# Kernel tuning notes

Measured on AMD Instinct MI355X. Metric: run time of the kernel, lower is better.

## Reference

```python
import jax, jax.numpy as jnp
import numpy as np

N_NODES, N_EDGES, B = 5000, 160000, 8
IN_DIM, NB, RH = 64, 8, 64
MUL0, MUL1, MUL2 = 32, 16, 8
NW = 144  # 32*3 + 16*2 + 8*2 tensor-product path weights per edge
R_MAX, AVG_NEI = 6.0, 32.0
NL, POOL_H, OUT_D = 4, 128, 512


def setup_inputs():
    ks = jax.random.split(jax.random.key(0), 24)
    f = lambda k, shape, scale=1.0: jax.random.normal(k, shape, jnp.float32) * scale
    return {
        "x": f(ks[0], (N_NODES, IN_DIM)),
        "pos": f(ks[1], (N_NODES, 3)),
        "W_in": f(ks[2], (IN_DIM, MUL0), IN_DIM ** -0.5),
        "Wr1": f(ks[3], (NL, NB, RH), NB ** -0.5), "br1": jnp.zeros((NL, RH)),
        "Wr2": f(ks[4], (NL, RH, RH), RH ** -0.5), "br2": jnp.zeros((NL, RH)),
        "Wr3": f(ks[5], (NL, RH, NW), RH ** -0.5), "br3": jnp.zeros((NL, NW)),
        "Wm0": f(ks[6], (NL, 56, MUL0), 56 ** -0.5),
        "Wm1": f(ks[7], (NL, 48, MUL1), 48 ** -0.5),
        "Wm2": f(ks[8], (NL, 40, MUL2), 40 ** -0.5),
        "Ws0": f(ks[9], (NL, MUL0, MUL0), MUL0 ** -0.5),
        "Ws1": f(ks[10], (NL, MUL1, MUL1), MUL1 ** -0.5),
        "Ws2": f(ks[11], (NL, MUL2, MUL2), MUL2 ** -0.5),
        "Wg": f(ks[12], (NL, MUL0, MUL1 + MUL2), MUL0 ** -0.5), "bg": jnp.zeros((NL, MUL1 + MUL2)),
        "Wp1": f(ks[13], (MUL0, POOL_H), MUL0 ** -0.5), "bp1": jnp.zeros((POOL_H,)),
        "Wp2": f(ks[14], (POOL_H, POOL_H), POOL_H ** -0.5), "bp2": jnp.zeros((POOL_H,)),
        "Wp3": f(ks[15], (POOL_H, 1), POOL_H ** -0.5), "bp3": jnp.zeros((1,)),
        "Wo1": f(ks[16], (MUL0, OUT_D * 2), MUL0 ** -0.5), "bo1": jnp.zeros((OUT_D * 2,)),
        "g1": jnp.ones((OUT_D * 2,)), "be1": jnp.zeros((OUT_D * 2,)),
        "Wo2": f(ks[17], (OUT_D * 2, OUT_D), (OUT_D * 2) ** -0.5), "bo2": jnp.zeros((OUT_D,)),
        "g2": jnp.ones((OUT_D,)), "be2": jnp.zeros((OUT_D,)),
        "edge_index": jax.random.randint(ks[18], (2, N_EDGES), 0, N_NODES),
        "batch": jnp.sort(jax.random.randint(ks[19], (N_NODES,), 0, B)),
    }


def _ln(x, gamma, beta):
    m = x.mean(-1, keepdims=True)
    v = x.var(-1, keepdims=True)
    return (x - m) / jnp.sqrt(v + 1e-5) * gamma + beta


def _forward(x, pos, W_in, Wr1, br1, Wr2, br2, Wr3, br3, Wm0, Wm1, Wm2,
             Ws0, Ws1, Ws2, Wg, bg, Wp1, bp1, Wp2, bp2, Wp3, bp3,
             Wo1, bo1, g1, be1, Wo2, bo2, g2, be2, edge_index, batch):
    N = x.shape[0]
    src, dst = edge_index[0], edge_index[1]
    vec = pos[src] - pos[dst]                       # [E,3]
    r = jnp.sqrt(jnp.sum(vec * vec, -1) + 1e-12)    # [E]
    u = vec / r[:, None]
    # Bessel radial basis with smooth polynomial cutoff (p=6)
    nfreq = jnp.arange(1, NB + 1, dtype=x.dtype)
    bess = jnp.sqrt(2.0 / R_MAX) * jnp.sin(nfreq * jnp.pi * r[:, None] / R_MAX) / r[:, None]
    t = jnp.clip(r / R_MAX, 0.0, 1.0)
    fcut = (1.0 - 28.0 * t**6 + 48.0 * t**7 - 21.0 * t**8) * (r < R_MAX).astype(x.dtype)
    edge_emb = bess * fcut[:, None]                 # [E,NB]
    # real spherical harmonics of edge direction, component normalization
    ux, uy, uz = u[:, 0], u[:, 1], u[:, 2]
    Y1 = jnp.sqrt(3.0) * u                          # [E,3]
    Y2 = jnp.stack([15.0**0.5 * ux * uy, 15.0**0.5 * uy * uz,
                    0.5 * 5.0**0.5 * (3.0 * uz * uz - 1.0),
                    15.0**0.5 * ux * uz, 0.5 * 15.0**0.5 * (ux * ux - uy * uy)], -1)  # [E,5]
    # input embedding: 64x0e -> hidden irreps (only scalar path exists; l>0 start at 0)
    s = x @ W_in                                    # [N,32]
    v = jnp.zeros((N, MUL1, 3), x.dtype)            # [N,16,3] 1o
    q = jnp.zeros((N, MUL2, 5), x.dtype)            # [N,8,5]  2e
    for i in range(NL):
        w = jax.nn.silu(edge_emb @ Wr1[i] + br1[i])
        w = jax.nn.silu(w @ Wr2[i] + br2[i])
        w = w @ Wr3[i] + br3[i]                     # [E,144] per-edge TP path weights
        w_ss, w_sv, w_sq, w_vs, w_vv, w_qs, w_qq = jnp.split(w, [32, 64, 96, 112, 128, 136], -1)
        se, ve, qe = s[src], v[src], q[src]         # gather
        # tensor-product messages, grouped by output irrep
        m0 = jnp.concatenate([w_ss * se,
                              w_vv * jnp.einsum('ecm,em->ec', ve, Y1) / 3.0**0.5,
                              w_qq * jnp.einsum('ecm,em->ec', qe, Y2) / 5.0**0.5], -1)   # [E,56]
        m1 = jnp.concatenate([(w_sv * se)[:, :, None] * Y1[:, None, :],
                              w_vs[:, :, None] * ve], 1)                                  # [E,48,3]
        m2 = jnp.concatenate([(w_sq * se)[:, :, None] * Y2[:, None, :],
                              w_qs[:, :, None] * qe], 1)                                  # [E,40,5]
        a0 = jax.ops.segment_sum(m0, dst, num_segments=N) / AVG_NEI
        a1 = jax.ops.segment_sum(m1, dst, num_segments=N) / AVG_NEI
        a2 = jax.ops.segment_sum(m2, dst, num_segments=N) / AVG_NEI
        # per-irrep linear mix + self-connection
        ns = a0 @ Wm0[i] + s @ Ws0[i]
        nv = jnp.einsum('ncm,co->nom', a1, Wm1[i]) + jnp.einsum('ncm,co->nom', v, Ws1[i])
        nq = jnp.einsum('ncm,co->nom', a2, Wm2[i]) + jnp.einsum('ncm,co->nom', q, Ws2[i])
        # gate activation + resnet
        gates = jax.nn.sigmoid(ns @ Wg[i] + bg[i])  # [N,24]
        s = s + jax.nn.silu(ns)
        v = v + nv * gates[:, :MUL1, None]
        q = q + nq * gates[:, MUL1:, None]
    # attention pooling over scalar channels (scatter-softmax per graph)
    logits = (jax.nn.silu(jax.nn.silu(s @ Wp1 + bp1) @ Wp2 + bp2) @ Wp3 + bp3)[:, 0]
    mx = jax.ops.segment_max(logits, batch, num_segments=B)
    z = jnp.exp(logits - mx[batch])
    att = z / jax.ops.segment_sum(z, batch, num_segments=B)[batch]
    gpool = jax.ops.segment_sum(s * att[:, None], batch, num_segments=B)  # [B,32]
    h = jax.nn.silu(_ln(gpool @ Wo1 + bo1, g1, be1))
    return _ln(h @ Wo2 + bo2, g2, be2)              # [B,512]


def reference(x, pos, W_in, Wr1, br1, Wr2, br2, Wr3, br3, Wm0, Wm1, Wm2,
              Ws0, Ws1, Ws2, Wg, bg, Wp1, bp1, Wp2, bp2, Wp3, bp3,
              Wo1, bo1, g1, be1, Wo2, bo2, g2, be2, edge_index, batch):
    return _forward(x, pos, W_in, Wr1, br1, Wr2, br2, Wr3, br3, Wm0, Wm1, Wm2,
                    Ws0, Ws1, Ws2, Wg, bg, Wp1, bp1, Wp2, bp2, Wp3, bp3,
                    Wo1, bo1, g1, be1, Wo2, bo2, g2, be2, edge_index, batch)
```

## Files before the change

### kernel.cpp

```cpp
#include <hip/hip_runtime.h>

constexpr int NN  = 5000;
constexpr int NE  = 160000;
constexpr int NB_ = 8;
constexpr float RMAX   = 6.0f;
constexpr float INV_AVG = 1.0f/32.0f;
constexpr float SQ3  = 1.7320508075688772f;
constexpr float ISQ3 = 0.5773502691896258f;
constexpr float ISQ5 = 0.4472135954999579f;
constexpr float SQ15 = 3.872983346207417f;
constexpr float SQ5  = 2.2360679774997896f;
constexpr float PIF  = 3.14159265358979323846f;

__device__ __forceinline__ float sigmoid_f(float x){
    return 1.0f / (1.0f + __expf(-x));
}
__device__ __forceinline__ float silu_f(float x){ return x * sigmoid_f(x); }

__global__ void k_geom(const float* __restrict__ pos, const int* __restrict__ ei,
                       float* __restrict__ geom, int* __restrict__ counts){
    int e = blockIdx.x*256 + threadIdx.x;
    if (e >= NE) return;
    int s = ei[e], d = ei[NE + e];
    float vx = pos[3*s]-pos[3*d], vy = pos[3*s+1]-pos[3*d+1], vz = pos[3*s+2]-pos[3*d+2];
    float r2 = vx*vx + vy*vy + vz*vz + 1e-12f;
    float r  = sqrtf(r2);
    float ir = 1.0f/r;
    float ux = vx*ir, uy = vy*ir, uz = vz*ir;
    float t  = fminf(r*(1.0f/RMAX), 1.0f);
    float t2=t*t, t3=t2*t, t6=t3*t3, t7=t6*t, t8=t7*t;
    float fc = (1.0f - 28.0f*t6 + 48.0f*t7 - 21.0f*t8) * (r < RMAX ? 1.0f : 0.0f);
    float cb = sqrtf(2.0f/RMAX) * ir * fc;
    float w[16];
    #pragma unroll
    for (int k=0;k<8;k++){
        float arg = (float)(k+1) * (PIF/RMAX) * r;
        w[k] = cb * sinf(arg);
    }
    w[8]  = SQ3*ux; w[9] = SQ3*uy; w[10] = SQ3*uz;
    w[11] = SQ15*ux*uy; w[12] = SQ15*uy*uz; w[13] = 0.5f*SQ5*(3.0f*uz*uz-1.0f);
    w[14] = SQ15*ux*uz; w[15] = 0.5f*SQ15*(ux*ux-uy*uy);
    float4* o = (float4*)(geom + (size_t)e*16);
    o[0] = make_float4(w[0],w[1],w[2],w[3]);
    o[1] = make_float4(w[4],w[5],w[6],w[7]);
    o[2] = make_float4(w[8],w[9],w[10],w[11]);
    o[3] = make_float4(w[12],w[13],w[14],w[15]);
    atomicAdd(&counts[d], 1);
}

__global__ void k_scan(int* __restrict__ cr, int* __restrict__ fpos){
    __shared__ int part[256];
    int t = threadIdx.x;
    const int CH = (NN + 255)/256;
    int base = t*CH;
    int s = 0;
    for (int i=0;i<CH;i++){ int idx = base+i; if (idx < NN) s += cr[idx]; }
    part[t] = s; __syncthreads();
    for (int off=1; off<256; off<<=1){
        int v = (t >= off) ? part[t-off] : 0;
        __syncthreads();
        part[t] += v;
        __syncthreads();
    }
    int run = (t==0) ? 0 : part[t-1];
    for (int i=0;i<CH;i++){
        int idx = base+i;
        if (idx < NN){
            int c = cr[idx];
            cr[idx]  = run;
            fpos[idx] = run;
            run += c;
        } else if (idx == NN){
            cr[idx] = run;
        }
    }
}

__global__ void k_fill(const int* __restrict__ ei, int* __restrict__ fpos,
                       int* __restrict__ elist, int* __restrict__ slot){
    int e = blockIdx.x*256 + threadIdx.x;
    if (e >= NE) return;
    int d = ei[NE+e];
    int p = atomicAdd(&fpos[d], 1);
    elist[p] = e;
    slot[e]  = p;
}

__global__ void k_sinit(const float* __restrict__ x, const float* __restrict__ Win,
                        float* __restrict__ sA){
    int tid = blockIdx.x*256 + threadIdx.x;
    int n = tid >> 5, o = tid & 31;
    if (n >= NN) return;
    float a = 0.f;
    #pragma unroll
    for (int k=0;k<64;k++) a = fmaf(x[n*64+k], Win[k*32+o], a);
    sA[n*32+o] = a;
}

__launch_bounds__(256)
__global__ void k_mlp(const float* __restrict__ geom, const int* __restrict__ slot,
                      const float* __restrict__ Wr1, const float* __restrict__ br1,
                      const float* __restrict__ Wr2, const float* __restrict__ br2,
                      const float* __restrict__ Wr3, const float* __restrict__ br3,
                      float* __restrict__ wbuf, int layer){
    __shared__ float w1s[8*64];
    __shared__ float w2s[64*64];
    __shared__ float w3s[64*144];
    __shared__ float b1s[64], b2s[64], b3s[144];
    __shared__ float embs[64][8];
    __shared__ float hs[64][68];
    __shared__ int   slots[64];

    const int t  = threadIdx.x;
    const int e0 = blockIdx.x * 64;
    const float* W1 = Wr1 + layer*(8*64);
    const float* b1 = br1 + layer*64;
    const float* W2 = Wr2 + layer*(64*64);
    const float* b2 = br2 + layer*64;
    const float* W3 = Wr3 + layer*(64*144);
    const float* b3 = br3 + layer*144;

    {
        const float4* W2v = (const float4*)W2;
        float4* w2v = (float4*)w2s;
        #pragma unroll
        for (int i=0;i<4;i++) w2v[t + 256*i] = W2v[t + 256*i];
        const float4* W3v = (const float4*)W3;
        float4* w3v = (float4*)w3s;
        #pragma unroll
        for (int i=0;i<9;i++) w3v[t + 256*i] = W3v[t + 256*i];
        if (t < 128) ((float4*)w1s)[t] = ((const float4*)W1)[t];
        if (t < 64){ b1s[t] = b1[t]; b2s[t] = b2[t]; slots[t] = slot[e0 + t]; }
        if (t < 144) b3s[t] = b3[t];
        if (t < 128){
            ((float4*)embs)[t] = *((const float4*)geom + (size_t)(e0 + (t>>1))*4 + (t&1));
        }
    }
    __syncthreads();

    const int eg = t >> 3;
    const int jg = t & 7;
    const int ea = eg*2, eb = ea+1;

    float a0[2][8];
    #pragma unroll
    for (int i=0;i<2;i++)
        #pragma unroll
        for (int u=0;u<8;u++) a0[i][u] = b1s[8*jg+u];
    #pragma unroll
    for (int k=0;k<8;k++){
        float e_a = embs[ea][k], e_b = embs[eb][k];
        #pragma unroll
        for (int u=0;u<8;u++){
            float wv = w1s[k*64 + 8*jg + u];
            a0[0][u] = fmaf(e_a, wv, a0[0][u]);
            a0[1][u] = fmaf(e_b, wv, a0[1][u]);
        }
    }
    #pragma unroll
    for (int i=0;i<2;i++){
        int e = ea + i;
        float4 p0 = make_float4(silu_f(a0[i][0]), silu_f(a0[i][1]), silu_f(a0[i][2]), silu_f(a0[i][3]));
        float4 p1 = make_float4(silu_f(a0[i][4]), silu_f(a0[i][5]), silu_f(a0[i][6]), silu_f(a0[i][7]));
        *(float4*)&hs[e][8*jg]     = p0;
        *(float4*)&hs[e][8*jg + 4] = p1;
    }
    __syncthreads();

    float a1[2][8];
    #pragma unroll
    for (int i=0;i<2;i++)
        #pragma unroll
        for (int u=0;u<8;u++) a1[i][u] = b2s[8*jg+u];
    #pragma unroll
    for (int k=0;k<64;k++){
        float h_a = hs[ea][k], h_b = hs[eb][k];
        float4 wA = *(const float4*)&w2s[k*64 + 8*jg];
        float4 wB = *(const float4*)&w2s[k*64 + 8*jg + 4];
        a1[0][0]=fmaf(h_a,wA.x,a1[0][0]); a1[0][1]=fmaf(h_a,wA.y,a1[0][1]);
        a1[0][2]=fmaf(h_a,wA.z,a1[0][2]); a1[0][3]=fmaf(h_a,wA.w,a1[0][3]);
        a1[0][4]=fmaf(h_a,wB.x,a1[0][4]); a1[0][5]=fmaf(h_a,wB.y,a1[0][5]);
        a1[0][6]=fmaf(h_a,wB.z,a1[0][6]); a1[0][7]=fmaf(h_a,wB.w,a1[0][7]);
        a1[1][0]=fmaf(h_b,wA.x,a1[1][0]); a1[1][1]=fmaf(h_b,wA.y,a1[1][1]);
        a1[1][2]=fmaf(h_b,wA.z,a1[1][2]); a1[1][3]=fmaf(h_b,wA.w,a1[1][3]);
        a1[1][4]=fmaf(h_b,wB.x,a1[1][4]); a1[1][5]=fmaf(h_b,wB.y,a1[1][5]);
        a1[1][6]=fmaf(h_b,wB.z,a1[1][6]); a1[1][7]=fmaf(h_b,wB.w,a1[1][7]);
    }
    __syncthreads();
    #pragma unroll
    for (int i=0;i<2;i++){
        int e = ea + i;
        float4 p0 = make_float4(silu_f(a1[i][0]), silu_f(a1[i][1]), silu_f(a1[i][2]), silu_f(a1[i][3]));
        float4 p1 = make_float4(silu_f(a1[i][4]), silu_f(a1[i][5]), silu_f(a1[i][6]), silu_f(a1[i][7]));
        *(float4*)&hs[e][8*jg]     = p0;
        *(float4*)&hs[e][8*jg + 4] = p1;
    }
    __syncthreads();

    float c2[2][18];
    #pragma unroll
    for (int i=0;i<2;i++)
        #pragma unroll
        for (int u=0;u<18;u++) c2[i][u] = b3s[18*jg+u];
    #pragma unroll
    for (int k=0;k<64;k++){
        float h_a = hs[ea][k], h_b = hs[eb][k];
        #pragma unroll
        for (int u2=0;u2<9;u2++){
            float2 wv = *(const float2*)&w3s[k*144 + 18*jg + 2*u2];
            c2[0][2*u2]   = fmaf(h_a, wv.x, c2[0][2*u2]);
            c2[0][2*u2+1] = fmaf(h_a, wv.y, c2[0][2*u2+1]);
            c2[1][2*u2]   = fmaf(h_b, wv.x, c2[1][2*u2]);
            c2[1][2*u2+1] = fmaf(h_b, wv.y, c2[1][2*u2+1]);
        }
    }
    #pragma unroll
    for (int i=0;i<2;i++){
        float* wo = wbuf + (size_t)slots[ea+i]*144 + 18*jg;
        #pragma unroll
        for (int u2=0;u2<9;u2++)
            *(float2*)(wo + 2*u2) = make_float2(c2[i][2*u2], c2[i][2*u2+1]);
    }
}

__launch_bounds__(64)
__global__ void k_gather(const int* __restrict__ rowp, const int* __restrict__ elist,
                         const int* __restrict__ ei, const float* __restrict__ geom,
                         const float* __restrict__ wbuf,
                         const float* __restrict__ s_in, const float* __restrict__ v_in,
                         const float* __restrict__ q_in,
                         float* __restrict__ s_out, float* __restrict__ v_out,
                         float* __restrict__ q_out,
                         const float* __restrict__ Wm0, const float* __restrict__ Wm1,
                         const float* __restrict__ Wm2,
                         const float* __restrict__ Ws0, const float* __restrict__ Ws1,
                         const float* __restrict__ Ws2,
                         const float* __restrict__ Wg, const float* __restrict__ bg,
                         int layer){
    constexpr int SH_W = 0, SH_Y = 144, SH_SE = 152, SH_VE = 184, SH_QE = 232, SH_ONE = 272;
    __shared__ float sh[273];
    __shared__ float lacc[400];
    __shared__ float lnode[120];
    __shared__ float lns[32];
    __shared__ float lgate[24];
    int n = blockIdx.x;
    int lane = threadIdx.x;
    if (lane < 32) lnode[lane]      = s_in[n*32+lane];
    if (lane < 48) lnode[32+lane]   = v_in[n*48+lane];
    if (lane < 40) lnode[80+lane]   = q_in[n*40+lane];
    if (lane == 0) sh[SH_ONE] = 1.0f;

    int typ[7], wiA[7], siA[7], yiA[7];
    #pragma unroll
    for (int t=0;t<7;t++){
        int c = lane + 64*t;
        int T=3, W=0, S=0, Y=SH_ONE;
        if (c < 32){ T=0; W=c; S=SH_SE+c; }
        else if (c < 48){ T=1; W=112+(c-32); S=SH_VE+3*(c-32); }
        else if (c < 56){ T=2; W=136+(c-48); S=SH_QE+5*(c-48); }
        else if (c < 200){
            int d=c-56; int row=d/3; int col=d-3*row;
            if (row < 32){ T=0; W=32+row;       S=SH_SE+row;              Y=SH_Y+col; }
            else         { T=0; W=96+(row-32);  S=SH_VE+3*(row-32)+col; }
        } else if (c < 400){
            int d=c-200; int row=d/5; int col=d-5*row;
            if (row < 32){ T=0; W=64+row;       S=SH_SE+row;              Y=SH_Y+3+col; }
            else         { T=0; W=128+(row-32); S=SH_QE+5*(row-32)+col; }
        }
        typ[t]=T; wiA[t]=W; siA[t]=S; yiA[t]=Y;
    }
    float acc[7];
    #pragma unroll
    for (int t=0;t<7;t++) acc[t]=0.f;

    int beg = rowp[n], end = rowp[n+1];
    for (int idx=beg; idx<end; ++idx){
        int e   = elist[idx];
        int src = ei[e];
        if (lane < 36){
            *(float4*)&sh[SH_W + lane*4] = *(const float4*)(wbuf + (size_t)idx*144 + lane*4);
        } else if (lane < 38){
            *(float4*)&sh[SH_Y + (lane-36)*4] = *(const float4*)(geom + (size_t)e*16 + 8 + (lane-36)*4);
        } else if (lane < 46){
            *(float4*)&sh[SH_SE + (lane-38)*4] = *(const float4*)(s_in + (size_t)src*32 + (lane-38)*4);
        } else if (lane < 58){
            *(float4*)&sh[SH_VE + (lane-46)*4] = *(const float4*)(v_in + (size_t)src*48 + (lane-46)*4);
        } else {
            *(float4*)&sh[SH_QE + (lane-58)*4] = *(const float4*)(q_in + (size_t)src*40 + (lane-58)*4);
        }
        if (lane < 4){
            *(float4*)&sh[SH_QE + 24 + lane*4] = *(const float4*)(q_in + (size_t)src*40 + 24 + lane*4);
        }
        __syncthreads();
        #pragma unroll
        for (int t=0;t<7;t++){
            float m;
            if (typ[t]==0)      m = sh[wiA[t]] * sh[siA[t]] * sh[yiA[t]];
            else if (typ[t]==1) m = sh[wiA[t]] * ISQ3 *
                                    (sh[siA[t]]*sh[SH_Y] + sh[siA[t]+1]*sh[SH_Y+1] + sh[siA[t]+2]*sh[SH_Y+2]);
            else if (typ[t]==2) m = sh[wiA[t]] * ISQ5 *
                                    (sh[siA[t]]*sh[SH_Y+3] + sh[siA[t]+1]*sh[SH_Y+4] + sh[siA[t]+2]*sh[SH_Y+5] +
                                     sh[siA[t]+3]*sh[SH_Y+6] + sh[siA[t]+4]*sh[SH_Y+7]);
            else                m = 0.f;
            acc[t] += m;
        }
        __syncthreads();
    }
    #pragma unroll
    for (int t=0;t<7;t++){
        int c = lane + 64*t;
        if (c < 400) lacc[c] = acc[t] * INV_AVG;
    }
    __syncthreads();

    const float* Wm0p = Wm0 + layer*(56*32);
    const float* Ws0p = Ws0 + layer*(32*32);
    const float* Wm1p = Wm1 + layer*(48*16);
    const float* Ws1p = Ws1 + layer*(16*16);
    const float* Wm2p = Wm2 + layer*(40*8);
    const float* Ws2p = Ws2 + layer*(8*8);
    const float* Wgp  = Wg  + layer*(32*24);
    const float* bgp  = bg  + layer*24;

    if (lane < 32){
        float a = 0.f;
        #pragma unroll
        for (int c=0;c<56;c++) a = fmaf(lacc[c],  Wm0p[c*32+lane], a);
        #pragma unroll
        for (int c=0;c<32;c++) a = fmaf(lnode[c], Ws0p[c*32+lane], a);
        lns[lane] = a;
    }
    int o3 = lane/3, m3 = lane - 3*o3;
    int o5 = lane/5, m5 = lane - 5*o5;
    float nv = 0.f, nq = 0.f;
    if (lane < 48){
        float a = 0.f;
        #pragma unroll
        for (int c=0;c<48;c++) a = fmaf(lacc[56+c*3+m3],   Wm1p[c*16+o3], a);
        #pragma unroll
        for (int c=0;c<16;c++) a = fmaf(lnode[32+c*3+m3],  Ws1p[c*16+o3], a);
        nv = a;
    }
    if (lane < 40){
        float a = 0.f;
        #pragma unroll
        for (int c=0;c<40;c++) a = fmaf(lacc[200+c*5+m5],  Wm2p[c*8+o5], a);
        #pragma unroll
        for (int c=0;c<8;c++)  a = fmaf(lnode[80+c*5+m5],  Ws2p[c*8+o5], a);
        nq = a;
    }
    __syncthreads();
    if (lane < 24){
        float a = bgp[lane];
        #pragma unroll
        for (int c=0;c<32;c++) a = fmaf(lns[c], Wgp[c*24+lane], a);
        lgate[lane] = sigmoid_f(a);
    }
    __syncthreads();
    if (lane < 32) s_out[n*32+lane] = lnode[lane]    + silu_f(lns[lane]);
    if (lane < 48) v_out[n*48+lane] = lnode[32+lane] + nv * lgate[o3];
    if (lane < 40) q_out[n*40+lane] = lnode[80+lane] + nq * lgate[16+o5];
}

__launch_bounds__(128)
__global__ void k_pool(const float* __restrict__ s_in,
                       const float* __restrict__ Wp1, const float* __restrict__ bp1,
                       const float* __restrict__ Wp2, const float* __restrict__ bp2,
                       const float* __restrict__ Wp3, const float* __restrict__ bp3,
                       float* __restrict__ logits){
    __shared__ float ls[32];
    __shared__ float lh[128];
    __shared__ float wred[2];
    int n = blockIdx.x, t = threadIdx.x;
    if (t < 32) ls[t] = s_in[n*32+t];
    __syncthreads();
    float a = bp1[t];
    #pragma unroll
    for (int c=0;c<32;c++) a = fmaf(ls[c], Wp1[c*128+t], a);
    lh[t] = silu_f(a);
    __syncthreads();
    float b = bp2[t];
    #pragma unroll
    for (int k=0;k<128;k++) b = fmaf(lh[k], Wp2[k*128+t], b);
    float p = silu_f(b) * Wp3[t];
    #pragma unroll
    for (int off=32; off>0; off>>=1) p += __shfl_down(p, off, 64);
    if ((t & 63) == 0) wred[t>>6] = p;
    __syncthreads();
    if (t == 0) logits[n] = wred[0] + wred[1] + bp3[0];
}

__global__ void k_bmax(const float* __restrict__ logits, const int* __restrict__ batch,
                       float* __restrict__ mx){
    __shared__ float red[256];
    int b = blockIdx.x, t = threadIdx.x;
    float m = -3.0e38f;
    for (int n=t; n<NN; n+=256) if (batch[n]==b) m = fmaxf(m, logits[n]);
    red[t] = m; __syncthreads();
    for (int s2=128; s2>0; s2>>=1){ if (t<s2) red[t] = fmaxf(red[t], red[t+s2]); __syncthreads(); }
    if (t==0) mx[b] = red[0];
}

__global__ void k_z(const float* __restrict__ logits, const int* __restrict__ batch,
                    const float* __restrict__ mx, float* __restrict__ zbuf,
                    float* __restrict__ denom){
    int n = blockIdx.x*256 + threadIdx.x;
    if (n >= NN) return;
    int b = batch[n];
    float z = __expf(logits[n] - mx[b]);
    zbuf[n] = z;
    atomicAdd(&denom[b], z);
}

__global__ void k_gpool(const float* __restrict__ s_in, const float* __restrict__ zbuf,
                        const int* __restrict__ batch, const float* __restrict__ denom,
                        float* __restrict__ gpool){
    __shared__ float red[8][32];
    int b = blockIdx.x, t = threadIdx.x;
    int c = t & 31, g = t >> 5;
    float a = 0.f;
    for (int n=g; n<NN; n+=8){
        if (batch[n]==b) a = fmaf(zbuf[n], s_in[n*32+c], a);
    }
    red[g][c] = a; __syncthreads();
    if (t < 32){
        float s2 = 0.f;
        #pragma unroll
        for (int g2=0; g2<8; g2++) s2 += red[g2][t];
        gpool[b*32+t] = s2 / denom[b];
    }
}

__launch_bounds__(1024)
__global__ void k_out1(const float* __restrict__ gpool, const float* __restrict__ Wo1,
                       const float* __restrict__ bo1, const float* __restrict__ g1,
                       const float* __restrict__ be1, float* __restrict__ hbuf){
    __shared__ float lg[32];
    __shared__ float red[1024];
    __shared__ float stats[2];
    int b = blockIdx.x, t = threadIdx.x;
    if (t < 32) lg[t] = gpool[b*32+t];
    __syncthreads();
    float a = bo1[t];
    #pragma unroll
    for (int c=0;c<32;c++) a = fmaf(lg[c], Wo1[c*1024+t], a);
    red[t] = a; __syncthreads();
    for (int s2=512; s2>0; s2>>=1){ if (t<s2) red[t]+=red[t+s2]; __syncthreads(); }
    if (t==0) stats[0] = red[0]*(1.0f/1024.0f);
    __syncthreads();
    float mean = stats[0];
    float d = a - mean;
    red[t] = d*d; __syncthreads();
    for (int s2=512; s2>0; s2>>=1){ if (t<s2) red[t]+=red[t+s2]; __syncthreads(); }
    if (t==0) stats[1] = red[0]*(1.0f/1024.0f);
    __syncthreads();
    float rstd = rsqrtf(stats[1] + 1e-5f);
    hbuf[b*1024+t] = silu_f(d*rstd*g1[t] + be1[t]);
}

__launch_bounds__(1024)
__global__ void k_out2(const float* __restrict__ hbuf, const float* __restrict__ Wo2,
                       const float* __restrict__ bo2, const float* __restrict__ g2,
                       const float* __restrict__ be2, float* __restrict__ out){
    __shared__ float lh[1024];
    __shared__ float part[1024];
    __shared__ float red[1024];
    __shared__ float stats[2];
    int b = blockIdx.x, t = threadIdx.x;
    lh[t] = hbuf[b*1024 + t];
    __syncthreads();
    int j = t & 511, half = t >> 9;
    float a = (half == 0) ? bo2[j] : 0.0f;
    int k0 = half*512;
    #pragma unroll 8
    for (int k=0;k<512;k++) a = fmaf(lh[k0+k], Wo2[(size_t)(k0+k)*512 + j], a);
    part[t] = a; __syncthreads();
    float y = 0.f;
    if (t < 512) y = part[t] + part[t+512];
    red[t] = (t < 512) ? y : 0.f; __syncthreads();
    for (int s2=512; s2>0; s2>>=1){ if (t<s2) red[t]+=red[t+s2]; __syncthreads(); }
    if (t==0) stats[0] = red[0]*(1.0f/512.0f);
    __syncthreads();
    float mean = stats[0];
    float d = y - mean;
    red[t] = (t < 512) ? d*d : 0.f; __syncthreads();
    for (int s2=512; s2>0; s2>>=1){ if (t<s2) red[t]+=red[t+s2]; __syncthreads(); }
    if (t==0) stats[1] = red[0]*(1.0f/512.0f);
    __syncthreads();
    float rstd = rsqrtf(stats[1] + 1e-5f);
    if (t < 512) out[b*512+t] = d*rstd*g2[t] + be2[t];
}

extern "C" void kernel_launch(void* const* d_in, const int* in_sizes, int n_in,
                              void* d_out, int out_size, void* d_ws, size_t ws_size,
                              hipStream_t stream){
    const float* x   = (const float*)d_in[0];
    const float* pos = (const float*)d_in[1];
    const float* Win = (const float*)d_in[2];
    const float* Wr1 = (const float*)d_in[3];
    const float* br1 = (const float*)d_in[4];
    const float* Wr2 = (const float*)d_in[5];
    const float* br2 = (const float*)d_in[6];
    const float* Wr3 = (const float*)d_in[7];
    const float* br3 = (const float*)d_in[8];
    const float* Wm0 = (const float*)d_in[9];
    const float* Wm1 = (const float*)d_in[10];
    const float* Wm2 = (const float*)d_in[11];
    const float* Ws0 = (const float*)d_in[12];
    const float* Ws1 = (const float*)d_in[13];
    const float* Ws2 = (const float*)d_in[14];
    const float* Wg  = (const float*)d_in[15];
    const float* bg  = (const float*)d_in[16];
    const float* Wp1 = (const float*)d_in[17];
    const float* bp1 = (const float*)d_in[18];
    const float* Wp2 = (const float*)d_in[19];
    const float* bp2 = (const float*)d_in[20];
    const float* Wp3 = (const float*)d_in[21];
    const float* bp3 = (const float*)d_in[22];
    const float* Wo1 = (const float*)d_in[23];
    const float* bo1 = (const float*)d_in[24];
    const float* g1  = (const float*)d_in[25];
    const float* be1 = (const float*)d_in[26];
    const float* Wo2 = (const float*)d_in[27];
    const float* bo2 = (const float*)d_in[28];
    const float* g2  = (const float*)d_in[29];
    const float* be2 = (const float*)d_in[30];
    const int* ei    = (const int*)d_in[31];
    const int* batch = (const int*)d_in[32];
    float* out = (float*)d_out;

    char* wsb = (char*)d_ws;
    size_t off = 0;
    auto take = [&](size_t bytes)->char*{
        char* p = wsb + off;
        off = (off + bytes + 255) & ~(size_t)255;
        return p;
    };
    float* geom  = (float*)take((size_t)NE*16*4);
    float* wbuf  = (float*)take((size_t)NE*144*4);
    int*   rowp  = (int*)take((size_t)(NN+1)*4);
    int*   fpos  = (int*)take((size_t)NN*4);
    int*   elist = (int*)take((size_t)NE*4);
    int*   slot  = (int*)take((size_t)NE*4);
    float* sA = (float*)take((size_t)NN*32*4);
    float* sB = (float*)take((size_t)NN*32*4);
    float* vA = (float*)take((size_t)NN*48*4);
    float* vB = (float*)take((size_t)NN*48*4);
    float* qA = (float*)take((size_t)NN*40*4);
    float* qB = (float*)take((size_t)NN*40*4);
    float* logits = (float*)take((size_t)NN*4);
    float* zbuf   = (float*)take((size_t)NN*4);
    float* mx     = (float*)take(64);
    float* denom  = (float*)take(64);
    float* gpool  = (float*)take((size_t)NB_*32*4);
    float* hbuf   = (float*)take((size_t)NB_*1024*4);
    (void)ws_size; (void)in_sizes; (void)n_in; (void)out_size;

    hipMemsetAsync(rowp, 0, (size_t)(NN+1)*4, stream);
    hipMemsetAsync(vA,   0, (size_t)NN*48*4, stream);
    hipMemsetAsync(qA,   0, (size_t)NN*40*4, stream);
    hipMemsetAsync(denom,0, 64, stream);

    k_geom<<<(NE+255)/256, 256, 0, stream>>>(pos, ei, geom, rowp);
    k_scan<<<1, 256, 0, stream>>>(rowp, fpos);
    k_fill<<<(NE+255)/256, 256, 0, stream>>>(ei, fpos, elist, slot);
    k_sinit<<<(NN*32+255)/256, 256, 0, stream>>>(x, Win, sA);

    float* si=sA; float* so=sB; float* vi=vA; float* vo=vB; float* qi=qA; float* qo=qB;
    for (int layer=0; layer<4; ++layer){
        k_mlp<<<NE/64, 256, 0, stream>>>(geom, slot, Wr1, br1, Wr2, br2, Wr3, br3, wbuf, layer);
        k_gather<<<NN, 64, 0, stream>>>(rowp, elist, ei, geom, wbuf, si, vi, qi, so, vo, qo,
                                        Wm0, Wm1, Wm2, Ws0, Ws1, Ws2, Wg, bg, layer);
        float* ts=si; si=so; so=ts;
        float* tv=vi; vi=vo; vo=tv;
        float* tq=qi; qi=qo; qo=tq;
    }
    k_pool<<<NN, 128, 0, stream>>>(si, Wp1, bp1, Wp2, bp2, Wp3, bp3, logits);
    k_bmax<<<NB_, 256, 0, stream>>>(logits, batch, mx);
    k_z<<<(NN+255)/256, 256, 0, stream>>>(logits, batch, mx, zbuf, denom);
    k_gpool<<<NB_, 256, 0, stream>>>(si, zbuf, batch, denom, gpool);
    k_out1<<<NB_, 1024, 0, stream>>>(gpool, Wo1, bo1, g1, be1, hbuf);
    k_out2<<<NB_, 1024, 0, stream>>>(hbuf, Wo2, bo2, g2, be2, out);
}
```

Baseline: 1.147 ms.

## Parallelize gather over four waves, stream W3 from global, use batch ranges for pooling

The per-node gather kernel now uses 256 threads, with four waves each taking every fourth incoming edge. Each lane computes its tensor-product paths straight from global memory, and the partial sums are reduced in shared memory. This removes the per-edge shared staging and the two barriers per edge. The edge MLP's last layer now reads W3 from global/L1 with one edge per four threads instead of staging 36KB in shared memory, which should raise occupancy. Segment ranges are precomputed from the sorted batch so the max and pooling kernels scan only their own segment, at the cost of an extra small kernel.

```diff
diff --git a/kernel.cpp b/kernel.cpp
--- a/kernel.cpp
+++ b/kernel.cpp
@@ -97,7 +97,7 @@
     sA[n*32+o] = a;
 }
 
-__launch_bounds__(256)
+__launch_bounds__(256, 4)
 __global__ void k_mlp(const float* __restrict__ geom, const int* __restrict__ slot,
                       const float* __restrict__ Wr1, const float* __restrict__ br1,
                       const float* __restrict__ Wr2, const float* __restrict__ br2,
@@ -105,8 +105,7 @@
                       float* __restrict__ wbuf, int layer){
     __shared__ float w1s[8*64];
     __shared__ float w2s[64*64];
-    __shared__ float w3s[64*144];
-    __shared__ float b1s[64], b2s[64], b3s[144];
+    __shared__ float b1s[64], b2s[64];
     __shared__ float embs[64][8];
     __shared__ float hs[64][68];
     __shared__ int   slots[64];
@@ -125,13 +124,8 @@
         float4* w2v = (float4*)w2s;
         #pragma unroll
         for (int i=0;i<4;i++) w2v[t + 256*i] = W2v[t + 256*i];
-        const float4* W3v = (const float4*)W3;
-        float4* w3v = (float4*)w3s;
-        #pragma unroll
-        for (int i=0;i<9;i++) w3v[t + 256*i] = W3v[t + 256*i];
         if (t < 128) ((float4*)w1s)[t] = ((const float4*)W1)[t];
         if (t < 64){ b1s[t] = b1[t]; b2s[t] = b2[t]; slots[t] = slot[e0 + t]; }
-        if (t < 144) b3s[t] = b3[t];
         if (t < 128){
             ((float4*)embs)[t] = *((const float4*)geom + (size_t)(e0 + (t>>1))*4 + (t&1));
         }
@@ -197,33 +191,38 @@
     }
     __syncthreads();
 
-    float c2[2][18];
-    #pragma unroll
-    for (int i=0;i<2;i++)
-        #pragma unroll
-        for (int u=0;u<18;u++) c2[i][u] = b3s[18*jg+u];
-    #pragma unroll
+    const int et = t >> 2;
+    const int cg = t & 3;
+    float c4[36];
+    {
+        const float4* b3v = (const float4*)(b3 + 36*cg);
+        #pragma unroll
+        for (int u4=0;u4<9;u4++){
+            float4 bv = b3v[u4];
+            c4[4*u4]=bv.x; c4[4*u4+1]=bv.y; c4[4*u4+2]=bv.z; c4[4*u4+3]=bv.w;
+        }
+    }
+    const float* W3c = W3 + 36*cg;
+    #pragma unroll 4
     for (int k=0;k<64;k++){
-        float h_a = hs[ea][k], h_b = hs[eb][k];
-        #pragma unroll
-        for (int u2=0;u2<9;u2++){
-            float2 wv = *(const float2*)&w3s[k*144 + 18*jg + 2*u2];
-            c2[0][2*u2]   = fmaf(h_a, wv.x, c2[0][2*u2]);
-            c2[0][2*u2+1] = fmaf(h_a, wv.y, c2[0][2*u2+1]);
-            c2[1][2*u2]   = fmaf(h_b, wv.x, c2[1][2*u2]);
-            c2[1][2*u2+1] = fmaf(h_b, wv.y, c2[1][2*u2+1]);
-        }
-    }
-    #pragma unroll
-    for (int i=0;i<2;i++){
-        float* wo = wbuf + (size_t)slots[ea+i]*144 + 18*jg;
-        #pragma unroll
-        for (int u2=0;u2<9;u2++)
-            *(float2*)(wo + 2*u2) = make_float2(c2[i][2*u2], c2[i][2*u2+1]);
-    }
-}
-
-__launch_bounds__(64)
+        float h = hs[et][k];
+        const float4* wr = (const float4*)(W3c + k*144);
+        #pragma unroll
+        for (int u4=0;u4<9;u4++){
+            float4 wv = wr[u4];
+            c4[4*u4]   = fmaf(h, wv.x, c4[4*u4]);
+            c4[4*u4+1] = fmaf(h, wv.y, c4[4*u4+1]);
+            c4[4*u4+2] = fmaf(h, wv.z, c4[4*u4+2]);
+            c4[4*u4+3] = fmaf(h, wv.w, c4[4*u4+3]);
+        }
+    }
+    float* wo = wbuf + (size_t)slots[et]*144 + 36*cg;
+    #pragma unroll
+    for (int u4=0;u4<9;u4++)
+        *(float4*)(wo + 4*u4) = make_float4(c4[4*u4], c4[4*u4+1], c4[4*u4+2], c4[4*u4+3]);
+}
+
+__launch_bounds__(256, 8)
 __global__ void k_gather(const int* __restrict__ rowp, const int* __restrict__ elist,
                          const int* __restrict__ ei, const float* __restrict__ geom,
                          const float* __restrict__ wbuf,
@@ -237,80 +236,110 @@
                          const float* __restrict__ Ws2,
                          const float* __restrict__ Wg, const float* __restrict__ bg,
                          int layer){
-    constexpr int SH_W = 0, SH_Y = 144, SH_SE = 152, SH_VE = 184, SH_QE = 232, SH_ONE = 272;
-    __shared__ float sh[273];
+    __shared__ float pacc[4][400];
     __shared__ float lacc[400];
-    __shared__ float lnode[120];
     __shared__ float lns[32];
     __shared__ float lgate[24];
-    int n = blockIdx.x;
-    int lane = threadIdx.x;
-    if (lane < 32) lnode[lane]      = s_in[n*32+lane];
-    if (lane < 48) lnode[32+lane]   = v_in[n*48+lane];
-    if (lane < 40) lnode[80+lane]   = q_in[n*40+lane];
-    if (lane == 0) sh[SH_ONE] = 1.0f;
-
-    int typ[7], wiA[7], siA[7], yiA[7];
-    #pragma unroll
-    for (int t=0;t<7;t++){
-        int c = lane + 64*t;
-        int T=3, W=0, S=0, Y=SH_ONE;
-        if (c < 32){ T=0; W=c; S=SH_SE+c; }
-        else if (c < 48){ T=1; W=112+(c-32); S=SH_VE+3*(c-32); }
-        else if (c < 56){ T=2; W=136+(c-48); S=SH_QE+5*(c-48); }
-        else if (c < 200){
-            int d=c-56; int row=d/3; int col=d-3*row;
-            if (row < 32){ T=0; W=32+row;       S=SH_SE+row;              Y=SH_Y+col; }
-            else         { T=0; W=96+(row-32);  S=SH_VE+3*(row-32)+col; }
-        } else if (c < 400){
-            int d=c-200; int row=d/5; int col=d-5*row;
-            if (row < 32){ T=0; W=64+row;       S=SH_SE+row;              Y=SH_Y+3+col; }
-            else         { T=0; W=128+(row-32); S=SH_QE+5*(row-32)+col; }
-        }
-        typ[t]=T; wiA[t]=W; siA[t]=S; yiA[t]=Y;
-    }
-    float acc[7];
-    #pragma unroll
-    for (int t=0;t<7;t++) acc[t]=0.f;
-
-    int beg = rowp[n], end = rowp[n+1];
-    for (int idx=beg; idx<end; ++idx){
+    const int n = blockIdx.x;
+    const int t = threadIdx.x;
+    const int w = t >> 6;
+    const int lane = t & 63;
+
+    int s0_w, s0_o, s0_ob;
+    if (lane < 32){ s0_w = lane;            s0_o = lane;          s0_ob = lane; }
+    else if (lane < 48){ s0_w = 112+(lane-32); s0_o = 3*(lane-32); s0_ob = lane; }
+    else if (lane < 56){ s0_w = 136+(lane-48); s0_o = 5*(lane-48); s0_ob = lane; }
+    else { int R = lane-56; s0_w = 32+R; s0_o = R; s0_ob = 56+3*R; }
+    int s1_w, s1_o, s1_ob;
+    if (lane < 24){ int R = lane+8; s1_w = 32+R; s1_o = R;     s1_ob = 56+3*R; }
+    else if (lane < 40){ int j = lane-24; s1_w = 96+j; s1_o = 3*j; s1_ob = 152+3*j; }
+    else { int R = lane-40; s1_w = 64+R; s1_o = R; s1_ob = 200+5*R; }
+    int s2_w, s2_o, s2_ob;
+    if (lane < 8){ int R = lane+24; s2_w = 64+R; s2_o = R;   s2_ob = 200+5*R; }
+    else { int j = lane-8; s2_w = 128+j; s2_o = 5*j; s2_ob = 360+5*j; }
+
+    float a0[3] = {0.f,0.f,0.f};
+    float a1[5] = {0.f,0.f,0.f,0.f,0.f};
+    float a2[5] = {0.f,0.f,0.f,0.f,0.f};
+
+    const int beg = rowp[n], end = rowp[n+1];
+    for (int idx = beg + w; idx < end; idx += 4){
         int e   = elist[idx];
         int src = ei[e];
-        if (lane < 36){
-            *(float4*)&sh[SH_W + lane*4] = *(const float4*)(wbuf + (size_t)idx*144 + lane*4);
-        } else if (lane < 38){
-            *(float4*)&sh[SH_Y + (lane-36)*4] = *(const float4*)(geom + (size_t)e*16 + 8 + (lane-36)*4);
-        } else if (lane < 46){
-            *(float4*)&sh[SH_SE + (lane-38)*4] = *(const float4*)(s_in + (size_t)src*32 + (lane-38)*4);
-        } else if (lane < 58){
-            *(float4*)&sh[SH_VE + (lane-46)*4] = *(const float4*)(v_in + (size_t)src*48 + (lane-46)*4);
-        } else {
-            *(float4*)&sh[SH_QE + (lane-58)*4] = *(const float4*)(q_in + (size_t)src*40 + (lane-58)*4);
-        }
-        if (lane < 4){
-            *(float4*)&sh[SH_QE + 24 + lane*4] = *(const float4*)(q_in + (size_t)src*40 + 24 + lane*4);
-        }
-        __syncthreads();
-        #pragma unroll
-        for (int t=0;t<7;t++){
-            float m;
-            if (typ[t]==0)      m = sh[wiA[t]] * sh[siA[t]] * sh[yiA[t]];
-            else if (typ[t]==1) m = sh[wiA[t]] * ISQ3 *
-                                    (sh[siA[t]]*sh[SH_Y] + sh[siA[t]+1]*sh[SH_Y+1] + sh[siA[t]+2]*sh[SH_Y+2]);
-            else if (typ[t]==2) m = sh[wiA[t]] * ISQ5 *
-                                    (sh[siA[t]]*sh[SH_Y+3] + sh[siA[t]+1]*sh[SH_Y+4] + sh[siA[t]+2]*sh[SH_Y+5] +
-                                     sh[siA[t]+3]*sh[SH_Y+6] + sh[siA[t]+4]*sh[SH_Y+7]);
-            else                m = 0.f;
-            acc[t] += m;
-        }
-        __syncthreads();
-    }
-    #pragma unroll
-    for (int t=0;t<7;t++){
-        int c = lane + 64*t;
-        if (c < 400) lacc[c] = acc[t] * INV_AVG;
-    }
+        const float* gp = geom + (size_t)e*16;
+        float4 y14 = *(const float4*)(gp + 8);
+        float4 y58 = *(const float4*)(gp + 12);
+        const float* wp = wbuf + (size_t)idx*144;
+        const float* sp = s_in + (size_t)src*32;
+        const float* vp = v_in + (size_t)src*48;
+        const float* qp = q_in + (size_t)src*40;
+        {
+            float wv = wp[s0_w];
+            if (lane < 32){
+                a0[0] = fmaf(wv, sp[s0_o], a0[0]);
+            } else if (lane < 48){
+                float dv = vp[s0_o]*y14.x + vp[s0_o+1]*y14.y + vp[s0_o+2]*y14.z;
+                a0[0] = fmaf(wv*ISQ3, dv, a0[0]);
+            } else if (lane < 56){
+                float dq = qp[s0_o]*y14.w + qp[s0_o+1]*y58.x + qp[s0_o+2]*y58.y
+                         + qp[s0_o+3]*y58.z + qp[s0_o+4]*y58.w;
+                a0[0] = fmaf(wv*ISQ5, dq, a0[0]);
+            } else {
+                float tmp = wv * sp[s0_o];
+                a0[0] = fmaf(tmp, y14.x, a0[0]);
+                a0[1] = fmaf(tmp, y14.y, a0[1]);
+                a0[2] = fmaf(tmp, y14.z, a0[2]);
+            }
+        }
+        {
+            float wv = wp[s1_w];
+            if (lane < 24){
+                float tmp = wv * sp[s1_o];
+                a1[0] = fmaf(tmp, y14.x, a1[0]);
+                a1[1] = fmaf(tmp, y14.y, a1[1]);
+                a1[2] = fmaf(tmp, y14.z, a1[2]);
+            } else if (lane < 40){
+                a1[0] = fmaf(wv, vp[s1_o],   a1[0]);
+                a1[1] = fmaf(wv, vp[s1_o+1], a1[1]);
+                a1[2] = fmaf(wv, vp[s1_o+2], a1[2]);
+            } else {
+                float tmp = wv * sp[s1_o];
+                a1[0] = fmaf(tmp, y14.w, a1[0]);
+                a1[1] = fmaf(tmp, y58.x, a1[1]);
+                a1[2] = fmaf(tmp, y58.y, a1[2]);
+                a1[3] = fmaf(tmp, y58.z, a1[3]);
+                a1[4] = fmaf(tmp, y58.w, a1[4]);
+            }
+        }
+        if (lane < 16){
+            float wv = wp[s2_w];
+            if (lane < 8){
+                float tmp = wv * sp[s2_o];
+                a2[0] = fmaf(tmp, y14.w, a2[0]);
+                a2[1] = fmaf(tmp, y58.x, a2[1]);
+                a2[2] = fmaf(tmp, y58.y, a2[2]);
+                a2[3] = fmaf(tmp, y58.z, a2[3]);
+                a2[4] = fmaf(tmp, y58.w, a2[4]);
+            } else {
+                a2[0] = fmaf(wv, qp[s2_o],   a2[0]);
+                a2[1] = fmaf(wv, qp[s2_o+1], a2[1]);
+                a2[2] = fmaf(wv, qp[s2_o+2], a2[2]);
+                a2[3] = fmaf(wv, qp[s2_o+3], a2[3]);
+                a2[4] = fmaf(wv, qp[s2_o+4], a2[4]);
+            }
+        }
+    }
+    pacc[w][s0_ob] = a0[0];
+    if (lane >= 56){ pacc[w][s0_ob+1] = a0[1]; pacc[w][s0_ob+2] = a0[2]; }
+    pacc[w][s1_ob] = a1[0]; pacc[w][s1_ob+1] = a1[1]; pacc[w][s1_ob+2] = a1[2];
+    if (lane >= 40){ pacc[w][s1_ob+3] = a1[3]; pacc[w][s1_ob+4] = a1[4]; }
+    if (lane < 16){
+        #pragma unroll
+        for (int u=0;u<5;u++) pacc[w][s2_ob+u] = a2[u];
+    }
+    __syncthreads();
+    for (int c=t; c<400; c+=256)
+        lacc[c] = (pacc[0][c]+pacc[1][c]+pacc[2][c]+pacc[3][c]) * INV_AVG;
     __syncthreads();
 
     const float* Wm0p = Wm0 + layer*(56*32);
@@ -322,44 +351,44 @@
     const float* Wgp  = Wg  + layer*(32*24);
     const float* bgp  = bg  + layer*24;
 
-    if (lane < 32){
+    float nvv = 0.f, nqv = 0.f;
+    if (t < 32){
         float a = 0.f;
         #pragma unroll
-        for (int c=0;c<56;c++) a = fmaf(lacc[c],  Wm0p[c*32+lane], a);
-        #pragma unroll
-        for (int c=0;c<32;c++) a = fmaf(lnode[c], Ws0p[c*32+lane], a);
-        lns[lane] = a;
-    }
-    int o3 = lane/3, m3 = lane - 3*o3;
-    int o5 = lane/5, m5 = lane - 5*o5;
-    float nv = 0.f, nq = 0.f;
-    if (lane < 48){
-        float a = 0.f;
-        #pragma unroll
-        for (int c=0;c<48;c++) a = fmaf(lacc[56+c*3+m3],   Wm1p[c*16+o3], a);
-        #pragma unroll
-        for (int c=0;c<16;c++) a = fmaf(lnode[32+c*3+m3],  Ws1p[c*16+o3], a);
-        nv = a;
-    }
-    if (lane < 40){
-        float a = 0.f;
-        #pragma unroll
-        for (int c=0;c<40;c++) a = fmaf(lacc[200+c*5+m5],  Wm2p[c*8+o5], a);
-        #pragma unroll
-        for (int c=0;c<8;c++)  a = fmaf(lnode[80+c*5+m5],  Ws2p[c*8+o5], a);
-        nq = a;
-    }
-    __syncthreads();
-    if (lane < 24){
-        float a = bgp[lane];
-        #pragma unroll
-        for (int c=0;c<32;c++) a = fmaf(lns[c], Wgp[c*24+lane], a);
-        lgate[lane] = sigmoid_f(a);
-    }
-    __syncthreads();
-    if (lane < 32) s_out[n*32+lane] = lnode[lane]    + silu_f(lns[lane]);
-    if (lane < 48) v_out[n*48+lane] = lnode[32+lane] + nv * lgate[o3];
-    if (lane < 40) q_out[n*40+lane] = lnode[80+lane] + nq * lgate[16+o5];
+        for (int c=0;c<56;c++) a = fmaf(lacc[c], Wm0p[c*32+t], a);
+        #pragma unroll
+        for (int c=0;c<32;c++) a = fmaf(s_in[n*32+c], Ws0p[c*32+t], a);
+        lns[t] = a;
+    } else if (t >= 64 && t < 112){
+        int o = t-64, o3 = o/3, m3 = o-3*o3;
+        #pragma unroll
+        for (int c=0;c<48;c++) nvv = fmaf(lacc[56+c*3+m3], Wm1p[c*16+o3], nvv);
+        #pragma unroll
+        for (int c=0;c<16;c++) nvv = fmaf(v_in[n*48+c*3+m3], Ws1p[c*16+o3], nvv);
+    } else if (t >= 128 && t < 168){
+        int o = t-128, o5 = o/5, m5 = o-5*o5;
+        #pragma unroll
+        for (int c=0;c<40;c++) nqv = fmaf(lacc[200+c*5+m5], Wm2p[c*8+o5], nqv);
+        #pragma unroll
+        for (int c=0;c<8;c++)  nqv = fmaf(q_in[n*40+c*5+m5], Ws2p[c*8+o5], nqv);
+    }
+    __syncthreads();
+    if (t < 24){
+        float a = bgp[t];
+        #pragma unroll
+        for (int c=0;c<32;c++) a = fmaf(lns[c], Wgp[c*24+t], a);
+        lgate[t] = sigmoid_f(a);
+    }
+    __syncthreads();
+    if (t < 32){
+        s_out[n*32+t] = s_in[n*32+t] + silu_f(lns[t]);
+    } else if (t >= 64 && t < 112){
+        int o = t-64;
+        v_out[n*48+o] = v_in[n*48+o] + nvv * lgate[o/3];
+    } else if (t >= 128 && t < 168){
+        int o = t-128;
+        q_out[n*40+o] = q_in[n*40+o] + nqv * lgate[16+o/5];
+    }
 }
 
 __launch_bounds__(128)
@@ -390,14 +419,24 @@
     if (t == 0) logits[n] = wred[0] + wred[1] + bp3[0];
 }
 
-__global__ void k_bmax(const float* __restrict__ logits, const int* __restrict__ batch,
-                       float* __restrict__ mx){
-    __shared__ float red[256];
+__global__ void k_ranges(const int* __restrict__ batch, int* __restrict__ rs, int* __restrict__ re){
+    int n = blockIdx.x*256 + threadIdx.x;
+    if (n >= NN) return;
+    int b = batch[n];
+    if (n == 0 || batch[n-1] != b) rs[b] = n;
+    if (n == NN-1 || batch[n+1] != b) re[b] = n+1;
+}
+
+__launch_bounds__(1024)
+__global__ void k_bmax(const float* __restrict__ logits, const int* __restrict__ rs,
+                       const int* __restrict__ re, float* __restrict__ mx){
+    __shared__ float red[1024];
     int b = blockIdx.x, t = threadIdx.x;
+    int lo = rs[b], hi = re[b];
     float m = -3.0e38f;
-    for (int n=t; n<NN; n+=256) if (batch[n]==b) m = fmaxf(m, logits[n]);
+    for (int n=lo+t; n<hi; n+=1024) m = fmaxf(m, logits[n]);
     red[t] = m; __syncthreads();
-    for (int s2=128; s2>0; s2>>=1){ if (t<s2) red[t] = fmaxf(red[t], red[t+s2]); __syncthreads(); }
+    for (int s2=512; s2>0; s2>>=1){ if (t<s2) red[t] = fmaxf(red[t], red[t+s2]); __syncthreads(); }
     if (t==0) mx[b] = red[0];
 }
 
@@ -412,21 +451,21 @@
     atomicAdd(&denom[b], z);
 }
 
+__launch_bounds__(1024)
 __global__ void k_gpool(const float* __restrict__ s_in, const float* __restrict__ zbuf,
-                        const int* __restrict__ batch, const float* __restrict__ denom,
-                        float* __restrict__ gpool){
-    __shared__ float red[8][32];
+                        const int* __restrict__ rs, const int* __restrict__ re,
+                        const float* __restrict__ denom, float* __restrict__ gpool){
+    __shared__ float red[32][32];
     int b = blockIdx.x, t = threadIdx.x;
     int c = t & 31, g = t >> 5;
+    int lo = rs[b], hi = re[b];
     float a = 0.f;
-    for (int n=g; n<NN; n+=8){
-        if (batch[n]==b) a = fmaf(zbuf[n], s_in[n*32+c], a);
-    }
+    for (int n=lo+g; n<hi; n+=32) a = fmaf(zbuf[n], s_in[n*32+c], a);
     red[g][c] = a; __syncthreads();
     if (t < 32){
         float s2 = 0.f;
         #pragma unroll
-        for (int g2=0; g2<8; g2++) s2 += red[g2][t];
+        for (int g2=0; g2<32; g2++) s2 += red[g2][t];
         gpool[b*32+t] = s2 / denom[b];
     }
 }
@@ -552,6 +591,8 @@
     float* zbuf   = (float*)take((size_t)NN*4);
     float* mx     = (float*)take(64);
     float* denom  = (float*)take(64);
+    int*   rs     = (int*)take(64);
+    int*   re     = (int*)take(64);
     float* gpool  = (float*)take((size_t)NB_*32*4);
     float* hbuf   = (float*)take((size_t)NB_*1024*4);
     (void)ws_size; (void)in_sizes; (void)n_in; (void)out_size;
@@ -560,25 +601,28 @@
     hipMemsetAsync(vA,   0, (size_t)NN*48*4, stream);
     hipMemsetAsync(qA,   0, (size_t)NN*40*4, stream);
     hipMemsetAsync(denom,0, 64, stream);
+    hipMemsetAsync(rs,   0, 64, stream);
+    hipMemsetAsync(re,   0, 64, stream);
 
     k_geom<<<(NE+255)/256, 256, 0, stream>>>(pos, ei, geom, rowp);
     k_scan<<<1, 256, 0, stream>>>(rowp, fpos);
     k_fill<<<(NE+255)/256, 256, 0, stream>>>(ei, fpos, elist, slot);
     k_sinit<<<(NN*32+255)/256, 256, 0, stream>>>(x, Win, sA);
+    k_ranges<<<(NN+255)/256, 256, 0, stream>>>(batch, rs, re);
 
     float* si=sA; float* so=sB; float* vi=vA; float* vo=vB; float* qi=qA; float* qo=qB;
     for (int layer=0; layer<4; ++layer){
         k_mlp<<<NE/64, 256, 0, stream>>>(geom, slot, Wr1, br1, Wr2, br2, Wr3, br3, wbuf, layer);
-        k_gather<<<NN, 64, 0, stream>>>(rowp, elist, ei, geom, wbuf, si, vi, qi, so, vo, qo,
-                                        Wm0, Wm1, Wm2, Ws0, Ws1, Ws2, Wg, bg, layer);
+        k_gather<<<NN, 256, 0, stream>>>(rowp, elist, ei, geom, wbuf, si, vi, qi, so, vo, qo,
+                                         Wm0, Wm1, Wm2, Ws0, Ws1, Ws2, Wg, bg, layer);
         float* ts=si; si=so; so=ts;
         float* tv=vi; vi=vo; vo=tv;
         float* tq=qi; qi=qo; qo=tq;
     }
     k_pool<<<NN, 128, 0, stream>>>(si, Wp1, bp1, Wp2, bp2, Wp3, bp3, logits);
-    k_bmax<<<NB_, 256, 0, stream>>>(logits, batch, mx);
+    k_bmax<<<NB_, 1024, 0, stream>>>(logits, rs, re, mx);
     k_z<<<(NN+255)/256, 256, 0, stream>>>(logits, batch, mx, zbuf, denom);
-    k_gpool<<<NB_, 256, 0, stream>>>(si, zbuf, batch, denom, gpool);
+    k_gpool<<<NB_, 1024, 0, stream>>>(si, zbuf, rs, re, denom, gpool);
     k_out1<<<NB_, 1024, 0, stream>>>(gpool, Wo1, bo1, g1, be1, hbuf);
     k_out2<<<NB_, 1024, 0, stream>>>(hbuf, Wo2, bo2, g2, be2, out);
 }
```

New measurement: 1.946 ms. 1.7x slower.
